# Performance work log

Measured on AMD Instinct MI355X. Metric: run time of the kernel, lower is better.

Reference implementation:

```python
import jax, jax.numpy as jnp
import numpy as np


def _xnor_quant_weight(w):
    # XnorBinaryLinear.quant_weight: row-center, sign-binarize, scale by
    # per-output-channel mean absolute value (STE in training; forward value
    # is sign(wc) * scale).
    wc = w - jnp.mean(w, axis=1, keepdims=True)          # [OC, IC]
    scale = jnp.mean(jnp.abs(wc), axis=1, keepdims=True)  # [OC, 1]
    return jnp.sign(wc) * scale


def setup_inputs() -> dict:
    key = jax.random.key(0)
    k1, k2, k3, k4 = jax.random.split(key, 4)
    OC = IC = 4096
    N_OUT = int(0.05 * IC)  # 204 outlier columns
    TOKENS = 4096
    x = jax.random.normal(k1, (TOKENS, IC), dtype=jnp.float32)
    weight = jax.random.normal(k2, (OC, IC), dtype=jnp.float32) * 0.02
    bias = jax.random.normal(k3, (OC,), dtype=jnp.float32) * 0.02
    outlier_weight = jax.random.normal(k4, (OC, N_OUT), dtype=jnp.float32) * 0.02
    outlier_columns_index = jnp.arange(N_OUT, dtype=jnp.int32)
    return {
        "x": x,
        "weight": weight,
        "bias": bias,
        "outlier_weight": outlier_weight,
        "outlier_columns_index": outlier_columns_index,
    }


def reference(x, weight, bias, outlier_weight, outlier_columns_index):
    # binarize_except_outliers: quantize dense weight, then overwrite the
    # outlier input-channel columns with the kept full-precision weights.
    wq = _xnor_quant_weight(weight)                      # [OC, IC]
    wq = wq.at[:, outlier_columns_index].set(outlier_weight)
    # F.linear(x, w, b) = x @ w.T + b
    return jnp.einsum("ti,oi->to", x, wq) + bias
```

## Files before the change

### kernel.cpp

```cpp
#include <hip/hip_runtime.h>

typedef __bf16 bf16;
typedef __bf16 bf16x8 __attribute__((ext_vector_type(8)));
typedef float  f32x4  __attribute__((ext_vector_type(4)));
typedef float  f32x16 __attribute__((ext_vector_type(16)));
typedef int    i32x4  __attribute__((ext_vector_type(4)));
typedef int    i32x16 __attribute__((ext_vector_type(16)));
typedef signed char i8;

#define OC_N   4096
#define IC_K   4096
#define TOKENS 4096
#define KC     256

__global__ __launch_bounds__(256) void prep_kernel(
    const float* __restrict__ w, const float* __restrict__ x,
    const float* __restrict__ ow, const int* __restrict__ idx,
    i8* __restrict__ wsgn, i8* __restrict__ xq,
    bf16* __restrict__ xo, bf16* __restrict__ wcorr,
    float* __restrict__ scale_arr, float* __restrict__ sx_arr, int n_out)
{
    __shared__ float red[8];
    const int row = blockIdx.x;
    const int t = threadIdx.x;
    const int lane = t & 63, wv = t >> 6;

    const float4* wr = (const float4*)(w + (size_t)row * IC_K);
    const float4* xr = (const float4*)(x + (size_t)row * IC_K);
    float4 v[4], u[4];
#pragma unroll
    for (int i = 0; i < 4; i++) v[i] = wr[i * 256 + t];
#pragma unroll
    for (int i = 0; i < 4; i++) u[i] = xr[i * 256 + t];

    float xg = 0.f, wg = 0.f, og = 0.f;
    if (t < n_out) {
        const int colg = idx[t];
        xg = x[(size_t)row * IC_K + colg];
        wg = w[(size_t)row * IC_K + colg];
        og = ow[(size_t)row * n_out + t];
    }

    float s = 0.f;
#pragma unroll
    for (int i = 0; i < 4; i++)
        s += v[i].x + v[i].y + v[i].z + v[i].w;
    for (int o = 32; o > 0; o >>= 1) s += __shfl_down(s, o, 64);
    if (lane == 0) red[wv] = s;
    __syncthreads();
    const float mean = (red[0] + red[1] + red[2] + red[3]) * (1.f / IC_K);

    float sa = 0.f;
#pragma unroll
    for (int i = 0; i < 4; i++) {
        sa += fabsf(v[i].x - mean) + fabsf(v[i].y - mean) +
              fabsf(v[i].z - mean) + fabsf(v[i].w - mean);
    }
    for (int o = 32; o > 0; o >>= 1) sa += __shfl_down(sa, o, 64);
    if (lane == 0) red[4 + wv] = sa;
    __syncthreads();
    const float scale = (red[4] + red[5] + red[6] + red[7]) * (1.f / IC_K);

    i8* srow = wsgn + (size_t)row * IC_K;
#pragma unroll
    for (int i = 0; i < 4; i++) {
        float c[4] = { v[i].x - mean, v[i].y - mean, v[i].z - mean, v[i].w - mean };
        char4 q;
        q.x = (i8)((c[0] > 0.f) - (c[0] < 0.f));
        q.y = (i8)((c[1] > 0.f) - (c[1] < 0.f));
        q.z = (i8)((c[2] > 0.f) - (c[2] < 0.f));
        q.w = (i8)((c[3] > 0.f) - (c[3] < 0.f));
        *(char4*)(srow + (size_t)(i * 256 + t) * 4) = q;
    }

    float mx = 0.f;
#pragma unroll
    for (int i = 0; i < 4; i++)
        mx = fmaxf(mx, fmaxf(fmaxf(fabsf(u[i].x), fabsf(u[i].y)),
                             fmaxf(fabsf(u[i].z), fabsf(u[i].w))));
    for (int o = 32; o > 0; o >>= 1) mx = fmaxf(mx, __shfl_down(mx, o, 64));
    if (lane == 0) red[wv] = mx;
    __syncthreads();
    const float maxv = fmaxf(fmaxf(red[0], red[1]), fmaxf(red[2], red[3]));
    const float inv = maxv > 0.f ? 127.f / maxv : 0.f;
    const float sxv = maxv > 0.f ? maxv * (1.f / 127.f) : 1.f;

    i8* xrow = xq + (size_t)row * IC_K;
#pragma unroll
    for (int i = 0; i < 4; i++) {
        char4 q;
        q.x = (i8)(int)rintf(u[i].x * inv);
        q.y = (i8)(int)rintf(u[i].y * inv);
        q.z = (i8)(int)rintf(u[i].z * inv);
        q.w = (i8)(int)rintf(u[i].w * inv);
        *(char4*)(xrow + (size_t)(i * 256 + t) * 4) = q;
    }
    if (t == 0) { scale_arr[row] = scale; sx_arr[row] = sxv; }

    if (t < n_out) {
        xo[(size_t)row * KC + t] = (bf16)xg;
        const float wc_ = wg - mean;
        const float sg = (wc_ > 0.f) ? 1.f : ((wc_ < 0.f) ? -1.f : 0.f);
        wcorr[(size_t)row * KC + t] = (bf16)(og - scale * sg);
    } else if (t < KC) {
        xo[(size_t)row * KC + t] = (bf16)0.f;
        wcorr[(size_t)row * KC + t] = (bf16)0.f;
    }
}

__device__ __forceinline__ void gload16(const void* g, void* l)
{
    __builtin_amdgcn_global_load_lds(
        (const __attribute__((address_space(1))) void*)g,
        (__attribute__((address_space(3))) void*)l, 16, 0, 0);
}

#define VMCNT(n) asm volatile("s_waitcnt vmcnt(" #n ")" ::: "memory")
#define SCHED0   __builtin_amdgcn_sched_barrier(0)
#define BAR      __builtin_amdgcn_s_barrier()

__global__ __launch_bounds__(512, 2) void gemm_kernel(
    const i8* __restrict__ A, const i8* __restrict__ B,
    const bf16* __restrict__ Axo, const bf16* __restrict__ Bwc,
    const float* __restrict__ sx, const float* __restrict__ scale,
    const float* __restrict__ bias, float* __restrict__ C)
{
    constexpr int K = IC_K, N = OC_N;
    __shared__ __align__(16) i8 ring[5][2][16384];

    const int tid  = threadIdx.x;
    const int lane = tid & 63;
    const int wave = tid >> 6;
    const int wm = wave >> 2, wn = wave & 3;
    const int m32 = lane & 31, kg = lane >> 5;

    const int bid = blockIdx.x;
    const int xcd = bid & 7, tix = bid >> 3;
    const int bm = (xcd >> 1) * 4 + (tix & 3);
    const int bn = (xcd & 1) * 8 + (tix >> 2);

    const int Q0 = tid, Q1 = 512 + tid;
    const int r0 = Q0 >> 2, r1 = Q1 >> 2;
    const int q0 = (Q0 & 3) ^ ((r0 >> 1) & 3);
    const int q1 = (Q1 & 3) ^ ((r1 >> 1) & 3);
    const int d0 = Q0 * 16, d1 = Q1 * 16;

    const i8* gA0 = A + (size_t)(bm * 256 + r0) * K + q0 * 16;
    const i8* gA1 = A + (size_t)(bm * 256 + r1) * K + q1 * 16;
    const i8* gB0 = B + (size_t)(bn * 256 + r0) * K + q0 * 16;
    const i8* gB1 = B + (size_t)(bn * 256 + r1) * K + q1 * 16;

    auto stage = [&](int c) {
        i8* bs = &ring[c % 5][0][0];
        const int ko = c * 64;
        gload16(gA0 + ko, bs + d0);
        gload16(gA1 + ko, bs + d1);
        gload16(gB0 + ko, bs + 16384 + d0);
        gload16(gB1 + ko, bs + 16384 + d1);
    };

    int offA[4][2], offB[2][2];
#pragma unroll
    for (int mi = 0; mi < 4; ++mi) {
        const int r = wm * 128 + mi * 32 + m32;
#pragma unroll
        for (int ks = 0; ks < 2; ++ks)
            offA[mi][ks] = r * 64 + ((ks * 2 + kg) ^ ((r >> 1) & 3)) * 16;
    }
#pragma unroll
    for (int ni = 0; ni < 2; ++ni) {
        const int r = wn * 64 + ni * 32 + m32;
#pragma unroll
        for (int ks = 0; ks < 2; ++ks)
            offB[ni][ks] = r * 64 + ((ks * 2 + kg) ^ ((r >> 1) & 3)) * 16;
    }

    i32x16 acc[4][2] = {};

    auto reads_i8 = [&](int c, i32x4 (&af)[4][2], i32x4 (&bfr)[2][2]) {
        const i8* sA = &ring[c % 5][0][0];
        const i8* sB = sA + 16384;
#pragma unroll
        for (int mi = 0; mi < 4; ++mi)
#pragma unroll
            for (int ks = 0; ks < 2; ++ks)
                af[mi][ks] = *(const i32x4*)(sA + offA[mi][ks]);
#pragma unroll
        for (int ni = 0; ni < 2; ++ni)
#pragma unroll
            for (int ks = 0; ks < 2; ++ks)
                bfr[ni][ks] = *(const i32x4*)(sB + offB[ni][ks]);
    };
    auto mfma_i8 = [&](i32x4 (&af)[4][2], i32x4 (&bfr)[2][2]) {
        __builtin_amdgcn_s_setprio(1);
#pragma unroll
        for (int ks = 0; ks < 2; ++ks)
#pragma unroll
            for (int mi = 0; mi < 4; ++mi)
#pragma unroll
                for (int ni = 0; ni < 2; ++ni)
                    acc[mi][ni] = __builtin_amdgcn_mfma_i32_32x32x32_i8(
                        af[mi][ks], bfr[ni][ks], acc[mi][ni], 0, 0, 0);
        __builtin_amdgcn_s_setprio(0);
    };

    stage(0); stage(1); stage(2); stage(3);
#pragma unroll 5
    for (int c = 0; c < 60; ++c) {
        VMCNT(12); BAR; SCHED0;
        i32x4 af[4][2], bfr[2][2];
        reads_i8(c, af, bfr);
        SCHED0;
        stage(c + 4);
        SCHED0;
        mfma_i8(af, bfr);
    }
    {
        i32x4 af[4][2], bfr[2][2];
        VMCNT(12); BAR; SCHED0; reads_i8(60, af, bfr); SCHED0; mfma_i8(af, bfr);
        VMCNT(8);  BAR; SCHED0; reads_i8(61, af, bfr); SCHED0; mfma_i8(af, bfr);
        VMCNT(4);  BAR; SCHED0; reads_i8(62, af, bfr); SCHED0; mfma_i8(af, bfr);
        VMCNT(0);  BAR; SCHED0; reads_i8(63, af, bfr); SCHED0; mfma_i8(af, bfr);
    }

    const int rbase = bm * 256 + wm * 128 + 4 * kg;
    const int cbase = bn * 256 + wn * 64 + m32;
    float scl2[2], bv2[2];
#pragma unroll
    for (int ni = 0; ni < 2; ++ni) {
        scl2[ni] = scale[cbase + ni * 32];
        bv2[ni]  = bias[cbase + ni * 32];
    }
    f32x16 facc[4][2];
#pragma unroll
    for (int mi = 0; mi < 4; ++mi)
#pragma unroll
        for (int r = 0; r < 16; ++r) {
            const float sxv = sx[rbase + mi * 32 + (r & 3) + 8 * (r >> 2)];
#pragma unroll
            for (int ni = 0; ni < 2; ++ni)
                facc[mi][ni][r] = (float)acc[mi][ni][r] * sxv * scl2[ni];
        }
    asm volatile("s_waitcnt vmcnt(0)" ::: "memory");
    BAR;

    const i8* cA0 = (const i8*)Axo + (size_t)(bm * 256 + r0) * (KC * 2) + q0 * 16;
    const i8* cA1 = (const i8*)Axo + (size_t)(bm * 256 + r1) * (KC * 2) + q1 * 16;
    const i8* cB0 = (const i8*)Bwc + (size_t)(bn * 256 + r0) * (KC * 2) + q0 * 16;
    const i8* cB1 = (const i8*)Bwc + (size_t)(bn * 256 + r1) * (KC * 2) + q1 * 16;
    auto stagec = [&](int c) {
        i8* bs = &ring[c % 5][0][0];
        const int ko = c * 64;
        gload16(cA0 + ko, bs + d0);
        gload16(cA1 + ko, bs + d1);
        gload16(cB0 + ko, bs + 16384 + d0);
        gload16(cB1 + ko, bs + 16384 + d1);
    };
    auto reads_bf = [&](int c, bf16x8 (&af)[4][2], bf16x8 (&bfr)[2][2]) {
        const i8* sA = &ring[c % 5][0][0];
        const i8* sB = sA + 16384;
#pragma unroll
        for (int mi = 0; mi < 4; ++mi)
#pragma unroll
            for (int ks = 0; ks < 2; ++ks)
                af[mi][ks] = *(const bf16x8*)(sA + offA[mi][ks]);
#pragma unroll
        for (int ni = 0; ni < 2; ++ni)
#pragma unroll
            for (int ks = 0; ks < 2; ++ks)
                bfr[ni][ks] = *(const bf16x8*)(sB + offB[ni][ks]);
    };
    auto mfma_bf = [&](bf16x8 (&af)[4][2], bf16x8 (&bfr)[2][2]) {
        __builtin_amdgcn_s_setprio(1);
#pragma unroll
        for (int ks = 0; ks < 2; ++ks)
#pragma unroll
            for (int mi = 0; mi < 4; ++mi)
#pragma unroll
                for (int ni = 0; ni < 2; ++ni)
                    facc[mi][ni] = __builtin_amdgcn_mfma_f32_32x32x16_bf16(
                        af[mi][ks], bfr[ni][ks], facc[mi][ni], 0, 0, 0);
        __builtin_amdgcn_s_setprio(0);
    };

    stagec(0); stagec(1); stagec(2);
#pragma unroll
    for (int c = 0; c < 5; ++c) {
        VMCNT(8); BAR; SCHED0;
        bf16x8 af[4][2], bfr[2][2];
        reads_bf(c, af, bfr);
        SCHED0;
        stagec(c + 3);
        SCHED0;
        mfma_bf(af, bfr);
    }
    {
        bf16x8 af[4][2], bfr[2][2];
        VMCNT(8); BAR; SCHED0; reads_bf(5, af, bfr); SCHED0; mfma_bf(af, bfr);
        VMCNT(4); BAR; SCHED0; reads_bf(6, af, bfr); SCHED0; mfma_bf(af, bfr);
        VMCNT(0); BAR; SCHED0; reads_bf(7, af, bfr); SCHED0; mfma_bf(af, bfr);
    }

#pragma unroll
    for (int mi = 0; mi < 4; ++mi)
#pragma unroll
        for (int r = 0; r < 16; ++r) {
            const int row = rbase + mi * 32 + (r & 3) + 8 * (r >> 2);
#pragma unroll
            for (int ni = 0; ni < 2; ++ni)
                C[(size_t)row * N + cbase + ni * 32] = facc[mi][ni][r] + bv2[ni];
        }
}

extern "C" void kernel_launch(void* const* d_in, const int* in_sizes, int n_in,
                              void* d_out, int out_size, void* d_ws, size_t ws_size,
                              hipStream_t stream)
{
    const float* x    = (const float*)d_in[0];
    const float* w    = (const float*)d_in[1];
    const float* bias = (const float*)d_in[2];
    const float* ow   = (const float*)d_in[3];
    const int*   idx  = (const int*)d_in[4];
    const int    n_out = in_sizes[4];
    float* out = (float*)d_out;

    char* ws = (char*)d_ws;
    i8*    xq    = (i8*)ws;
    i8*    wsgn  = (i8*)(ws + (size_t)16 * 1024 * 1024);
    bf16*  xo    = (bf16*)(ws + (size_t)32 * 1024 * 1024);
    bf16*  wcorr = (bf16*)(ws + (size_t)34 * 1024 * 1024);
    float* sx    = (float*)(ws + (size_t)36 * 1024 * 1024);
    float* scl   = (float*)(ws + (size_t)36 * 1024 * 1024 + 16 * 1024);

    hipLaunchKernelGGL(prep_kernel, dim3(OC_N), dim3(256), 0, stream,
                       w, x, ow, idx, wsgn, xq, xo, wcorr, scl, sx, n_out);
    hipLaunchKernelGGL(gemm_kernel, dim3(256), dim3(512), 0, stream,
                       xq, wsgn, xo, wcorr, sx, scl, bias, out);
}
```

Baseline: 252.7 us.

## Pack binary weight signs to 2 bits and unpack in registers via v_perm

The prep kernel now stores the sign weights as 2-bit codes in a pre-swizzled chunk-major layout, so the B operand takes a quarter of the bytes in global memory and LDS. The GEMM loads packed B with only half the waves, reads 4-byte words from LDS, and expands them to int8 with bit tricks and a v_perm lookup before the MFMAs. The LDS ring shrinks per stage, and the correction GEMM is re-ringed to 3 buffers with per-wave vmcnt counts adjusted. The aim is to cut B memory traffic and LDS reads, at the cost of extra VALU unpack work inside the MFMA loop.

```diff
diff --git a/kernel.cpp b/kernel.cpp
--- a/kernel.cpp
+++ b/kernel.cpp
@@ -7,6 +7,7 @@
 typedef int    i32x4  __attribute__((ext_vector_type(4)));
 typedef int    i32x16 __attribute__((ext_vector_type(16)));
 typedef signed char i8;
+typedef unsigned int u32;
 
 #define OC_N   4096
 #define IC_K   4096
@@ -16,7 +17,7 @@
 __global__ __launch_bounds__(256) void prep_kernel(
     const float* __restrict__ w, const float* __restrict__ x,
     const float* __restrict__ ow, const int* __restrict__ idx,
-    i8* __restrict__ wsgn, i8* __restrict__ xq,
+    i8* __restrict__ wsgn2, i8* __restrict__ xq,
     bf16* __restrict__ xo, bf16* __restrict__ wcorr,
     float* __restrict__ scale_arr, float* __restrict__ sx_arr, int n_out)
 {
@@ -61,16 +62,22 @@
     __syncthreads();
     const float scale = (red[4] + red[5] + red[6] + red[7]) * (1.f / IC_K);
 
-    i8* srow = wsgn + (size_t)row * IC_K;
-#pragma unroll
-    for (int i = 0; i < 4; i++) {
-        float c[4] = { v[i].x - mean, v[i].y - mean, v[i].z - mean, v[i].w - mean };
-        char4 q;
-        q.x = (i8)((c[0] > 0.f) - (c[0] < 0.f));
-        q.y = (i8)((c[1] > 0.f) - (c[1] < 0.f));
-        q.z = (i8)((c[2] > 0.f) - (c[2] < 0.f));
-        q.w = (i8)((c[3] > 0.f) - (c[3] < 0.f));
-        *(char4*)(srow + (size_t)(i * 256 + t) * 4) = q;
+    {
+        const int swzr = (row >> 3) & 3;
+#pragma unroll
+        for (int i = 0; i < 4; i++) {
+            const float c0 = v[i].x - mean, c1 = v[i].y - mean;
+            const float c2 = v[i].z - mean, c3 = v[i].w - mean;
+            const int s0 = (c0 > 0.f) - (c0 < 0.f);
+            const int s1 = (c1 > 0.f) - (c1 < 0.f);
+            const int s2 = (c2 > 0.f) - (c2 < 0.f);
+            const int s3 = (c3 > 0.f) - (c3 < 0.f);
+            const unsigned pb = (unsigned)(s0 & 3) | ((unsigned)(s1 & 3) << 2) |
+                                ((unsigned)(s2 & 3) << 4) | ((unsigned)(s3 & 3) << 6);
+            const int cch  = i * 16 + (t >> 4);
+            const int slot = ((t >> 2) & 3) ^ swzr;
+            wsgn2[((size_t)cch * 4096 + row) * 16 + slot * 4 + (t & 3)] = (i8)pb;
+        }
     }
 
     float mx = 0.f;
@@ -120,13 +127,13 @@
 #define BAR      __builtin_amdgcn_s_barrier()
 
 __global__ __launch_bounds__(512, 2) void gemm_kernel(
-    const i8* __restrict__ A, const i8* __restrict__ B,
+    const i8* __restrict__ A, const i8* __restrict__ Bp,
     const bf16* __restrict__ Axo, const bf16* __restrict__ Bwc,
     const float* __restrict__ sx, const float* __restrict__ scale,
     const float* __restrict__ bias, float* __restrict__ C)
 {
     constexpr int K = IC_K, N = OC_N;
-    __shared__ __align__(16) i8 ring[5][2][16384];
+    __shared__ __align__(16) i8 ring[5 * 20480];
 
     const int tid  = threadIdx.x;
     const int lane = tid & 63;
@@ -147,19 +154,18 @@
 
     const i8* gA0 = A + (size_t)(bm * 256 + r0) * K + q0 * 16;
     const i8* gA1 = A + (size_t)(bm * 256 + r1) * K + q1 * 16;
-    const i8* gB0 = B + (size_t)(bn * 256 + r0) * K + q0 * 16;
-    const i8* gB1 = B + (size_t)(bn * 256 + r1) * K + q1 * 16;
+    const i8* gB2 = Bp + ((size_t)bn * 256 + tid) * 16;
 
     auto stage = [&](int c) {
-        i8* bs = &ring[c % 5][0][0];
+        i8* bs = ring + (c % 5) * 20480;
         const int ko = c * 64;
         gload16(gA0 + ko, bs + d0);
         gload16(gA1 + ko, bs + d1);
-        gload16(gB0 + ko, bs + 16384 + d0);
-        gload16(gB1 + ko, bs + 16384 + d1);
-    };
-
-    int offA[4][2], offB[2][2];
+        if (wave < 4)
+            gload16(gB2 + (size_t)c * 65536, bs + 16384 + tid * 16);
+    };
+
+    int offA[4][2];
 #pragma unroll
     for (int mi = 0; mi < 4; ++mi) {
         const int r = wm * 128 + mi * 32 + m32;
@@ -167,18 +173,22 @@
         for (int ks = 0; ks < 2; ++ks)
             offA[mi][ks] = r * 64 + ((ks * 2 + kg) ^ ((r >> 1) & 3)) * 16;
     }
+    int offB[2][2], offB2[2][2];
 #pragma unroll
     for (int ni = 0; ni < 2; ++ni) {
         const int r = wn * 64 + ni * 32 + m32;
 #pragma unroll
-        for (int ks = 0; ks < 2; ++ks)
-            offB[ni][ks] = r * 64 + ((ks * 2 + kg) ^ ((r >> 1) & 3)) * 16;
-    }
-
+        for (int ks = 0; ks < 2; ++ks) {
+            offB[ni][ks]  = r * 64 + ((ks * 2 + kg) ^ ((r >> 1) & 3)) * 16;
+            offB2[ni][ks] = r * 16 + (((ks * 2 + kg) ^ ((r >> 3) & 3)) * 4);
+        }
+    }
+
+    const unsigned lutv = 0xFF000100u;
     i32x16 acc[4][2] = {};
 
-    auto reads_i8 = [&](int c, i32x4 (&af)[4][2], i32x4 (&bfr)[2][2]) {
-        const i8* sA = &ring[c % 5][0][0];
+    auto loads_i8 = [&](int c, i32x4 (&af)[4][2], u32 (&pw)[2][2]) {
+        const i8* sA = ring + (c % 5) * 20480;
         const i8* sB = sA + 16384;
 #pragma unroll
         for (int mi = 0; mi < 4; ++mi)
@@ -189,9 +199,25 @@
         for (int ni = 0; ni < 2; ++ni)
 #pragma unroll
             for (int ks = 0; ks < 2; ++ks)
-                bfr[ni][ks] = *(const i32x4*)(sB + offB[ni][ks]);
-    };
-    auto mfma_i8 = [&](i32x4 (&af)[4][2], i32x4 (&bfr)[2][2]) {
+                pw[ni][ks] = *(const u32*)(sB + offB2[ni][ks]);
+    };
+    auto mfma_i8 = [&](i32x4 (&af)[4][2], u32 (&pw)[2][2]) {
+        i32x4 bfr[2][2];
+#pragma unroll
+        for (int ni = 0; ni < 2; ++ni)
+#pragma unroll
+            for (int ks = 0; ks < 2; ++ks) {
+                const unsigned p = pw[ni][ks];
+#pragma unroll
+                for (int k = 0; k < 4; ++k) {
+                    unsigned t2 = (p >> (8 * k)) & 0xFFu;
+                    t2 = (t2 | (t2 << 12)) & 0x000F000Fu;
+                    t2 = (t2 | (t2 << 6))  & 0x03030303u;
+                    unsigned r;
+                    asm("v_perm_b32 %0, %1, %1, %2" : "=v"(r) : "v"(lutv), "v"(t2));
+                    bfr[ni][ks][k] = (int)r;
+                }
+            }
         __builtin_amdgcn_s_setprio(1);
 #pragma unroll
         for (int ks = 0; ks < 2; ++ks)
@@ -207,20 +233,25 @@
     stage(0); stage(1); stage(2); stage(3);
 #pragma unroll 5
     for (int c = 0; c < 60; ++c) {
-        VMCNT(12); BAR; SCHED0;
-        i32x4 af[4][2], bfr[2][2];
-        reads_i8(c, af, bfr);
+        if (wave < 4) { VMCNT(9); } else { VMCNT(6); }
+        BAR; SCHED0;
+        i32x4 af[4][2]; u32 pw[2][2];
+        loads_i8(c, af, pw);
         SCHED0;
         stage(c + 4);
         SCHED0;
-        mfma_i8(af, bfr);
+        mfma_i8(af, pw);
     }
     {
-        i32x4 af[4][2], bfr[2][2];
-        VMCNT(12); BAR; SCHED0; reads_i8(60, af, bfr); SCHED0; mfma_i8(af, bfr);
-        VMCNT(8);  BAR; SCHED0; reads_i8(61, af, bfr); SCHED0; mfma_i8(af, bfr);
-        VMCNT(4);  BAR; SCHED0; reads_i8(62, af, bfr); SCHED0; mfma_i8(af, bfr);
-        VMCNT(0);  BAR; SCHED0; reads_i8(63, af, bfr); SCHED0; mfma_i8(af, bfr);
+        i32x4 af[4][2]; u32 pw[2][2];
+        if (wave < 4) { VMCNT(9); } else { VMCNT(6); }
+        BAR; SCHED0; loads_i8(60, af, pw); SCHED0; mfma_i8(af, pw);
+        if (wave < 4) { VMCNT(6); } else { VMCNT(4); }
+        BAR; SCHED0; loads_i8(61, af, pw); SCHED0; mfma_i8(af, pw);
+        if (wave < 4) { VMCNT(3); } else { VMCNT(2); }
+        BAR; SCHED0; loads_i8(62, af, pw); SCHED0; mfma_i8(af, pw);
+        VMCNT(0);
+        BAR; SCHED0; loads_i8(63, af, pw); SCHED0; mfma_i8(af, pw);
     }
 
     const int rbase = bm * 256 + wm * 128 + 4 * kg;
@@ -249,7 +280,7 @@
     const i8* cB0 = (const i8*)Bwc + (size_t)(bn * 256 + r0) * (KC * 2) + q0 * 16;
     const i8* cB1 = (const i8*)Bwc + (size_t)(bn * 256 + r1) * (KC * 2) + q1 * 16;
     auto stagec = [&](int c) {
-        i8* bs = &ring[c % 5][0][0];
+        i8* bs = ring + (c % 3) * 32768;
         const int ko = c * 64;
         gload16(cA0 + ko, bs + d0);
         gload16(cA1 + ko, bs + d1);
@@ -257,7 +288,7 @@
         gload16(cB1 + ko, bs + 16384 + d1);
     };
     auto reads_bf = [&](int c, bf16x8 (&af)[4][2], bf16x8 (&bfr)[2][2]) {
-        const i8* sA = &ring[c % 5][0][0];
+        const i8* sA = ring + (c % 3) * 32768;
         const i8* sB = sA + 16384;
 #pragma unroll
         for (int mi = 0; mi < 4; ++mi)
@@ -283,20 +314,19 @@
         __builtin_amdgcn_s_setprio(0);
     };
 
-    stagec(0); stagec(1); stagec(2);
-#pragma unroll
-    for (int c = 0; c < 5; ++c) {
-        VMCNT(8); BAR; SCHED0;
+    stagec(0); stagec(1);
+#pragma unroll
+    for (int c = 0; c < 6; ++c) {
+        VMCNT(4); BAR; SCHED0;
         bf16x8 af[4][2], bfr[2][2];
         reads_bf(c, af, bfr);
         SCHED0;
-        stagec(c + 3);
+        stagec(c + 2);
         SCHED0;
         mfma_bf(af, bfr);
     }
     {
         bf16x8 af[4][2], bfr[2][2];
-        VMCNT(8); BAR; SCHED0; reads_bf(5, af, bfr); SCHED0; mfma_bf(af, bfr);
         VMCNT(4); BAR; SCHED0; reads_bf(6, af, bfr); SCHED0; mfma_bf(af, bfr);
         VMCNT(0); BAR; SCHED0; reads_bf(7, af, bfr); SCHED0; mfma_bf(af, bfr);
     }
@@ -326,14 +356,14 @@
 
     char* ws = (char*)d_ws;
     i8*    xq    = (i8*)ws;
-    i8*    wsgn  = (i8*)(ws + (size_t)16 * 1024 * 1024);
-    bf16*  xo    = (bf16*)(ws + (size_t)32 * 1024 * 1024);
-    bf16*  wcorr = (bf16*)(ws + (size_t)34 * 1024 * 1024);
-    float* sx    = (float*)(ws + (size_t)36 * 1024 * 1024);
-    float* scl   = (float*)(ws + (size_t)36 * 1024 * 1024 + 16 * 1024);
+    i8*    wsgn2 = (i8*)(ws + (size_t)16 * 1024 * 1024);
+    bf16*  xo    = (bf16*)(ws + (size_t)20 * 1024 * 1024);
+    bf16*  wcorr = (bf16*)(ws + (size_t)22 * 1024 * 1024);
+    float* sx    = (float*)(ws + (size_t)24 * 1024 * 1024);
+    float* scl   = (float*)(ws + (size_t)24 * 1024 * 1024 + 16 * 1024);
 
     hipLaunchKernelGGL(prep_kernel, dim3(OC_N), dim3(256), 0, stream,
-                       w, x, ow, idx, wsgn, xq, xo, wcorr, scl, sx, n_out);
+                       w, x, ow, idx, wsgn2, xq, xo, wcorr, scl, sx, n_out);
     hipLaunchKernelGGL(gemm_kernel, dim3(256), dim3(512), 0, stream,
-                       xq, wsgn, xo, wcorr, sx, scl, bias, out);
+                       xq, wsgn2, xo, wcorr, sx, scl, bias, out);
 }
```

Result: no change. 256.4 us (+1.4%).

## Replace five-deep LDS ring with double-buffered two-chunk super-stages

Applied to the files above, without the earlier changes.

Both the int8 main loop and the bf16 correction loop switch from a 5-slot ring (4 chunks prefetched, partial vmcnt waits) to two 32KB-per-operand slots. Each slot holds two 64-wide K chunks, and each iteration waits for all loads (vmcnt 0). The aim is to halve the number of barriers per K and cut LDS footprint from 160KB to 128KB. In exchange, prefetch depth drops to one super-stage ahead, so global load latency is less hidden behind MFMA work.

```diff
diff --git a/kernel.cpp b/kernel.cpp
--- a/kernel.cpp
+++ b/kernel.cpp
@@ -126,7 +126,7 @@
     const float* __restrict__ bias, float* __restrict__ C)
 {
     constexpr int K = IC_K, N = OC_N;
-    __shared__ __align__(16) i8 ring[5][2][16384];
+    __shared__ __align__(16) i8 ring[2][2][32768];
 
     const int tid  = threadIdx.x;
     const int lane = tid & 63;
@@ -150,13 +150,17 @@
     const i8* gB0 = B + (size_t)(bn * 256 + r0) * K + q0 * 16;
     const i8* gB1 = B + (size_t)(bn * 256 + r1) * K + q1 * 16;
 
-    auto stage = [&](int c) {
-        i8* bs = &ring[c % 5][0][0];
-        const int ko = c * 64;
-        gload16(gA0 + ko, bs + d0);
-        gload16(gA1 + ko, bs + d1);
-        gload16(gB0 + ko, bs + 16384 + d0);
-        gload16(gB1 + ko, bs + 16384 + d1);
+    auto stage_super = [&](int s) {
+        i8* aslot = &ring[s & 1][0][0];
+        i8* bslot = &ring[s & 1][1][0];
+#pragma unroll
+        for (int h = 0; h < 2; ++h) {
+            const int ko = (2 * s + h) * 64;
+            gload16(gA0 + ko, aslot + h * 16384 + d0);
+            gload16(gA1 + ko, aslot + h * 16384 + d1);
+            gload16(gB0 + ko, bslot + h * 16384 + d0);
+            gload16(gB1 + ko, bslot + h * 16384 + d1);
+        }
     };
 
     int offA[4][2], offB[2][2];
@@ -177,9 +181,9 @@
 
     i32x16 acc[4][2] = {};
 
-    auto reads_i8 = [&](int c, i32x4 (&af)[4][2], i32x4 (&bfr)[2][2]) {
-        const i8* sA = &ring[c % 5][0][0];
-        const i8* sB = sA + 16384;
+    auto reads_i8 = [&](int s, int h, i32x4 (&af)[4][2], i32x4 (&bfr)[2][2]) {
+        const i8* sA = &ring[s & 1][0][h * 16384];
+        const i8* sB = &ring[s & 1][1][h * 16384];
 #pragma unroll
         for (int mi = 0; mi < 4; ++mi)
 #pragma unroll
@@ -204,23 +208,26 @@
         __builtin_amdgcn_s_setprio(0);
     };
 
-    stage(0); stage(1); stage(2); stage(3);
-#pragma unroll 5
-    for (int c = 0; c < 60; ++c) {
-        VMCNT(12); BAR; SCHED0;
+    stage_super(0);
+    for (int s = 0; s < 31; ++s) {
+        VMCNT(0); BAR; SCHED0;
         i32x4 af[4][2], bfr[2][2];
-        reads_i8(c, af, bfr);
-        SCHED0;
-        stage(c + 4);
+        reads_i8(s, 0, af, bfr);
+        SCHED0;
+        stage_super(s + 1);
         SCHED0;
         mfma_i8(af, bfr);
+        SCHED0;
+        reads_i8(s, 1, af, bfr);
+        SCHED0;
+        mfma_i8(af, bfr);
     }
     {
+        VMCNT(0); BAR; SCHED0;
         i32x4 af[4][2], bfr[2][2];
-        VMCNT(12); BAR; SCHED0; reads_i8(60, af, bfr); SCHED0; mfma_i8(af, bfr);
-        VMCNT(8);  BAR; SCHED0; reads_i8(61, af, bfr); SCHED0; mfma_i8(af, bfr);
-        VMCNT(4);  BAR; SCHED0; reads_i8(62, af, bfr); SCHED0; mfma_i8(af, bfr);
-        VMCNT(0);  BAR; SCHED0; reads_i8(63, af, bfr); SCHED0; mfma_i8(af, bfr);
+        reads_i8(31, 0, af, bfr); SCHED0; mfma_i8(af, bfr);
+        SCHED0;
+        reads_i8(31, 1, af, bfr); SCHED0; mfma_i8(af, bfr);
     }
 
     const int rbase = bm * 256 + wm * 128 + 4 * kg;
@@ -248,17 +255,21 @@
     const i8* cA1 = (const i8*)Axo + (size_t)(bm * 256 + r1) * (KC * 2) + q1 * 16;
     const i8* cB0 = (const i8*)Bwc + (size_t)(bn * 256 + r0) * (KC * 2) + q0 * 16;
     const i8* cB1 = (const i8*)Bwc + (size_t)(bn * 256 + r1) * (KC * 2) + q1 * 16;
-    auto stagec = [&](int c) {
-        i8* bs = &ring[c % 5][0][0];
-        const int ko = c * 64;
-        gload16(cA0 + ko, bs + d0);
-        gload16(cA1 + ko, bs + d1);
-        gload16(cB0 + ko, bs + 16384 + d0);
-        gload16(cB1 + ko, bs + 16384 + d1);
-    };
-    auto reads_bf = [&](int c, bf16x8 (&af)[4][2], bf16x8 (&bfr)[2][2]) {
-        const i8* sA = &ring[c % 5][0][0];
-        const i8* sB = sA + 16384;
+    auto stagec_super = [&](int s) {
+        i8* aslot = &ring[s & 1][0][0];
+        i8* bslot = &ring[s & 1][1][0];
+#pragma unroll
+        for (int h = 0; h < 2; ++h) {
+            const int ko = (2 * s + h) * 64;
+            gload16(cA0 + ko, aslot + h * 16384 + d0);
+            gload16(cA1 + ko, aslot + h * 16384 + d1);
+            gload16(cB0 + ko, bslot + h * 16384 + d0);
+            gload16(cB1 + ko, bslot + h * 16384 + d1);
+        }
+    };
+    auto reads_bf = [&](int s, int h, bf16x8 (&af)[4][2], bf16x8 (&bfr)[2][2]) {
+        const i8* sA = &ring[s & 1][0][h * 16384];
+        const i8* sB = &ring[s & 1][1][h * 16384];
 #pragma unroll
         for (int mi = 0; mi < 4; ++mi)
 #pragma unroll
@@ -283,22 +294,26 @@
         __builtin_amdgcn_s_setprio(0);
     };
 
-    stagec(0); stagec(1); stagec(2);
-#pragma unroll
-    for (int c = 0; c < 5; ++c) {
-        VMCNT(8); BAR; SCHED0;
+    stagec_super(0);
+    for (int s = 0; s < 3; ++s) {
+        VMCNT(0); BAR; SCHED0;
         bf16x8 af[4][2], bfr[2][2];
-        reads_bf(c, af, bfr);
-        SCHED0;
-        stagec(c + 3);
+        reads_bf(s, 0, af, bfr);
+        SCHED0;
+        stagec_super(s + 1);
         SCHED0;
         mfma_bf(af, bfr);
+        SCHED0;
+        reads_bf(s, 1, af, bfr);
+        SCHED0;
+        mfma_bf(af, bfr);
     }
     {
+        VMCNT(0); BAR; SCHED0;
         bf16x8 af[4][2], bfr[2][2];
-        VMCNT(8); BAR; SCHED0; reads_bf(5, af, bfr); SCHED0; mfma_bf(af, bfr);
-        VMCNT(4); BAR; SCHED0; reads_bf(6, af, bfr); SCHED0; mfma_bf(af, bfr);
-        VMCNT(0); BAR; SCHED0; reads_bf(7, af, bfr); SCHED0; mfma_bf(af, bfr);
+        reads_bf(3, 0, af, bfr); SCHED0; mfma_bf(af, bfr);
+        SCHED0;
+        reads_bf(3, 1, af, bfr); SCHED0; mfma_bf(af, bfr);
     }
 
 #pragma unroll
```

New measurement: 255.6 us. About the same (+1.1%).
